# Kernel tuning notes

Hardware: AMD Instinct MI355X
Metric: run time of the kernel (lower is better)

Reference implementation:

```python
import jax, jax.numpy as jnp
import numpy as np

N = 100000   # nodes
E = 1600000  # edges
D = 128      # input_dim == hidden_dim
L = 3        # n_layers
P = 7        # n_properties
B = 64       # graphs in batch
BN_EPS = 1e-5
NEG_SLOPE = 0.2


def setup_inputs() -> dict:
    key = jax.random.key(0)
    ks = jax.random.split(key, 18)
    s = 1.0 / np.sqrt(D)
    sp = 1.0 / np.sqrt(P)
    return {
        "x": jax.random.normal(ks[0], (N, D), jnp.float32),
        "edge_index": jax.random.randint(ks[1], (2, E), 0, N, dtype=jnp.int64),
        "batch": jnp.sort(jax.random.randint(ks[2], (N,), 0, B, dtype=jnp.int64)),
        "graph_stats": jax.random.normal(ks[3], (B, P), jnp.float32),
        # GIN MLP params (stacked over layers; input_dim == hidden_dim == D)
        "W1s": jax.random.normal(ks[4], (L, D, D), jnp.float32) * s,
        "b1s": jnp.zeros((L, D), jnp.float32),
        "gammas": jnp.ones((L, D), jnp.float32),
        "betas": jnp.zeros((L, D), jnp.float32),
        "bn_means": jax.random.normal(ks[5], (L, D), jnp.float32) * 0.1,
        "bn_vars": jax.random.uniform(ks[6], (L, D), jnp.float32) + 0.5,
        "W2s": jax.random.normal(ks[7], (L, D, D), jnp.float32) * s,
        "b2s": jnp.zeros((L, D), jnp.float32),
        # stat conditioning transforms
        "statWs": jax.random.normal(ks[8], (L, P, D), jnp.float32) * sp,
        "statBs": jnp.zeros((L, D), jnp.float32),
        # fc_out
        "fcW": jax.random.normal(ks[9], (D, D), jnp.float32) * s,
        "fcB": jnp.zeros((D,), jnp.float32),
    }


def reference(x, edge_index, batch, graph_stats,
              W1s, b1s, gammas, betas, bn_means, bn_vars, W2s, b2s,
              statWs, statBs, fcW, fcB):
    # per-node graph stats (nan -> -100, then broadcast by graph id)
    node_stats = jnp.nan_to_num(graph_stats, nan=-100.0)[batch]  # [N, P]
    src, dst = edge_index[0], edge_index[1]
    h = x
    for i in range(L):
        # GIN aggregation (eps = 0): (1+eps)*h_i + sum_{j->i} h_j
        agg = jax.ops.segment_sum(h[src], dst, num_segments=N)  # [N, D]
        m = h + agg
        # MLP: Linear -> LeakyReLU(0.2) -> BatchNorm1d (eval) -> Linear -> LeakyReLU(0.2)
        m = jax.nn.leaky_relu(m @ W1s[i] + b1s[i], NEG_SLOPE)
        m = (m - bn_means[i]) * (gammas[i] / jnp.sqrt(bn_vars[i] + BN_EPS)) + betas[i]
        m = jax.nn.leaky_relu(m @ W2s[i] + b2s[i], NEG_SLOPE)
        # stats conditioning add (dropout is identity in eval mode)
        h = m + node_stats @ statWs[i] + statBs[i]
    return h @ fcW + fcB  # [N, D]
```

## Files before the change

### kernel.cpp

```cpp
#include <hip/hip_runtime.h>
#include <math.h>

#define N_NODES 100000
#define N_EDGES 1600000
#define D 128
#define L_LAYERS 3
#define P_STATS 7
#define B_GRAPHS 64
#define BN_EPS 1e-5f
#define NEG_SLOPE 0.2f

#define NB 196
#define BCAP 10240
#define EPB 6400

typedef __attribute__((ext_vector_type(8))) short bf16x8;
typedef __attribute__((ext_vector_type(4))) float f32x4;

static __device__ __forceinline__ short f2bf(float f) {
    union { float f; unsigned u; } v;
    v.f = f;
    unsigned r = v.u + 0x7fffu + ((v.u >> 16) & 1u);
    return (short)(r >> 16);
}

static __device__ __forceinline__ float bf2f(short s) {
    union { unsigned u; float f; } v;
    v.u = ((unsigned)(unsigned short)s) << 16;
    return v.f;
}


__global__ void zero_n_kernel(int* __restrict__ p, int n) {
    int i = blockIdx.x * blockDim.x + threadIdx.x;
    if (i < n) p[i] = 0;
}

__global__ __launch_bounds__(256) void bucketA_kernel(const int* __restrict__ src,
                                                      const int* __restrict__ dst,
                                                      int* __restrict__ bucket_cnt,
                                                      int2* __restrict__ bucketbuf) {
    __shared__ int s_src[EPB];
    __shared__ int s_dst[EPB];
    __shared__ int hist[NB], base[NB], loc[NB];
    const int tid = threadIdx.x;
    const int e0 = blockIdx.x * EPB;
    for (int i = tid; i < NB; i += 256) { hist[i] = 0; loc[i] = 0; }
    __syncthreads();
    for (int i = tid; i < EPB; i += 256) {
        int s = src[e0 + i];
        int d = dst[e0 + i];
        s_src[i] = s;
        s_dst[i] = d;
        atomicAdd(&hist[d >> 9], 1);
    }
    __syncthreads();
    for (int i = tid; i < NB; i += 256)
        base[i] = hist[i] ? atomicAdd(&bucket_cnt[i], hist[i]) : 0;
    __syncthreads();
    for (int i = tid; i < EPB; i += 256) {
        int d = s_dst[i];
        int b = d >> 9;
        int off = atomicAdd(&loc[b], 1);
        int idx = base[b] + off;
        if (idx < BCAP) bucketbuf[(size_t)b * BCAP + idx] = make_int2(s_src[i], d);
    }
}

__global__ __launch_bounds__(256) void bucketB1_kernel(const int* __restrict__ bucket_cnt,
                                                       const int2* __restrict__ bucketbuf,
                                                       int* __restrict__ deg) {
    __shared__ int hist[512];
    const int b = blockIdx.x;
    for (int i = threadIdx.x; i < 512; i += 256) hist[i] = 0;
    __syncthreads();
    int cnt = min(bucket_cnt[b], BCAP);
    for (int i = threadIdx.x; i < cnt; i += 256) {
        int d = bucketbuf[(size_t)b * BCAP + i].y;
        atomicAdd(&hist[d & 511], 1);
    }
    __syncthreads();
    int nbase = b << 9;
    for (int i = threadIdx.x; i < 512; i += 256) {
        int node = nbase + i;
        if (node < N_NODES) deg[node] = hist[i];
    }
}

__global__ __launch_bounds__(256) void bucketB2_kernel(const int* __restrict__ bucket_cnt,
                                                       const int2* __restrict__ bucketbuf,
                                                       int* __restrict__ cursor,
                                                       int* __restrict__ csr_src) {
    const int b = blockIdx.x;
    int cnt = min(bucket_cnt[b], BCAP);
    for (int i = threadIdx.x; i < cnt; i += 256) {
        int2 p = bucketbuf[(size_t)b * BCAP + i];
        int pos = atomicAdd(&cursor[p.y], 1);
        csr_src[pos] = p.x;
    }
}


__global__ void scan1_kernel(const int* __restrict__ deg, int* __restrict__ incl,
                             int* __restrict__ bsum) {
    __shared__ int s[256];
    const int tid = threadIdx.x;
    const int base = blockIdx.x * 2048;
    int v[8];
    int sum = 0;
    const int idx0 = base + tid * 8;
#pragma unroll
    for (int i = 0; i < 8; ++i) {
        int idx = idx0 + i;
        int d = (idx < N_NODES) ? deg[idx] : 0;
        sum += d;
        v[i] = sum;
    }
    s[tid] = sum;
    __syncthreads();
    for (int off = 1; off < 256; off <<= 1) {
        int t = (tid >= off) ? s[tid - off] : 0;
        __syncthreads();
        s[tid] += t;
        __syncthreads();
    }
    int prev = (tid > 0) ? s[tid - 1] : 0;
#pragma unroll
    for (int i = 0; i < 8; ++i) {
        int idx = idx0 + i;
        if (idx < N_NODES) incl[idx] = v[i] + prev;
    }
    if (tid == 255) bsum[blockIdx.x] = s[255];
}

__global__ void scan2_kernel(int* __restrict__ bsum, int nb) {
    if (threadIdx.x == 0 && blockIdx.x == 0) {
        int run = 0;
        for (int i = 0; i < nb; ++i) { int t = bsum[i]; bsum[i] = run; run += t; }
    }
}

__global__ void scan3_kernel(const int* __restrict__ deg, const int* __restrict__ incl,
                             const int* __restrict__ bsum, int* __restrict__ start,
                             int* __restrict__ cursor) {
    int i = blockIdx.x * blockDim.x + threadIdx.x;
    if (i < N_NODES) {
        int inc = incl[i] + bsum[i >> 11];
        int st = inc - deg[i];
        start[i] = st;
        cursor[i] = st;
    }
    if (i == 0) start[N_NODES] = N_EDGES;
}

__global__ void gproj_kernel(const float* __restrict__ gs, const float* __restrict__ statWs,
                             const float* __restrict__ statBs, float* __restrict__ gproj) {
    int b = blockIdx.x;
    int l = blockIdx.y;
    int j = threadIdx.x;
    float acc = statBs[l * D + j];
#pragma unroll
    for (int p = 0; p < P_STATS; ++p) {
        float g = gs[b * P_STATS + p];
        if (g != g) g = -100.0f;
        acc += g * statWs[(l * P_STATS + p) * D + j];
    }
    gproj[(l * B_GRAPHS + b) * D + j] = acc;
}

__global__ void wconv_kernel(const float* __restrict__ W1s, const float* __restrict__ W2s,
                             const float* __restrict__ fcW, short* __restrict__ wt) {
    int mid = blockIdx.y;
    const float* src = (mid < 3) ? (W1s + mid * D * D)
                                 : ((mid < 6) ? (W2s + (mid - 3) * D * D) : fcW);
    short* dstm = wt + mid * D * D;
    int i = blockIdx.x * 256 + threadIdx.x;
    int k = i >> 7, n = i & 127;
    dstm[n * D + k] = f2bf(src[i]);
}

__global__ __launch_bounds__(256) void xconv_kernel(const float* __restrict__ x,
                                                    short* __restrict__ xb) {
    int i = blockIdx.x * 256 + threadIdx.x;
    const float4* x4 = (const float4*)x;
    float4 a = x4[i * 2], b = x4[i * 2 + 1];
    short s[8];
    s[0] = f2bf(a.x); s[1] = f2bf(a.y); s[2] = f2bf(a.z); s[3] = f2bf(a.w);
    s[4] = f2bf(b.x); s[5] = f2bf(b.y); s[6] = f2bf(b.z); s[7] = f2bf(b.w);
    *(bf16x8*)&xb[i * 8] = *(bf16x8*)s;
}

__global__ __launch_bounds__(256) void agg_kernel(const short* __restrict__ hb,
                                                  const int* __restrict__ start,
                                                  const int* __restrict__ csr_src,
                                                  short* __restrict__ m_bf) {
    int node = blockIdx.x * 16 + (threadIdx.x >> 4);
    int c8 = threadIdx.x & 15;
    const bf16x8* h8 = (const bf16x8*)hb;

    bf16x8 own = h8[node * 16 + c8];
    float acc[8];
#pragma unroll
    for (int i = 0; i < 8; ++i) acc[i] = bf2f(own[i]);

    int s = start[node];
    int e = start[node + 1];
    int k = s;
    for (; k + 4 <= e; k += 4) {
        int sn0 = csr_src[k];
        int sn1 = csr_src[k + 1];
        int sn2 = csr_src[k + 2];
        int sn3 = csr_src[k + 3];
        bf16x8 v0 = h8[sn0 * 16 + c8];
        bf16x8 v1 = h8[sn1 * 16 + c8];
        bf16x8 v2 = h8[sn2 * 16 + c8];
        bf16x8 v3 = h8[sn3 * 16 + c8];
#pragma unroll
        for (int i = 0; i < 8; ++i) acc[i] += bf2f(v0[i]);
#pragma unroll
        for (int i = 0; i < 8; ++i) acc[i] += bf2f(v1[i]);
#pragma unroll
        for (int i = 0; i < 8; ++i) acc[i] += bf2f(v2[i]);
#pragma unroll
        for (int i = 0; i < 8; ++i) acc[i] += bf2f(v3[i]);
    }
    for (; k < e; ++k) {
        int sn0 = csr_src[k];
        bf16x8 v0 = h8[sn0 * 16 + c8];
#pragma unroll
        for (int i = 0; i < 8; ++i) acc[i] += bf2f(v0[i]);
    }

    short pk[8];
#pragma unroll
    for (int i = 0; i < 8; ++i) pk[i] = f2bf(acc[i]);
    *(bf16x8*)&m_bf[node * D + c8 * 8] = *(bf16x8*)pk;
}

template <bool FUSE_FC>
__global__ __launch_bounds__(256, 4) void mlp_mfma_kernel(
    const short* __restrict__ m_bf,
    const short* __restrict__ W1t,
    const float* __restrict__ b1,
    const float* __restrict__ gamma, const float* __restrict__ beta,
    const float* __restrict__ mean, const float* __restrict__ var,
    const short* __restrict__ W2t,
    const float* __restrict__ b2,
    const float* __restrict__ gproj, const int* __restrict__ batch,
    const short* __restrict__ Wft, const float* __restrict__ fcb,
    float* __restrict__ outf, short* __restrict__ outb) {
    __shared__ short sy[64 * 128];
    __shared__ float sB1[128], sSc[128], sSb[128], sB2[128], sFC[128];

    const int tid = threadIdx.x;
    const int wid = tid >> 6;
    const int lane = tid & 63;
    const int lr = lane & 15;
    const int lk = lane >> 4;

    if (tid < 128) {
        sB1[tid] = b1[tid];
        float sc = gamma[tid] * rsqrtf(var[tid] + BN_EPS);
        sSc[tid] = sc;
        sSb[tid] = beta[tid] - mean[tid] * sc;
        sB2[tid] = b2[tid];
        if (FUSE_FC) sFC[tid] = fcb[tid];
    }
    __syncthreads();

    const int nlBase = (wid >> 1) * 32;
    const int nodeBase = blockIdx.x * 64 + nlBase;
    const int featBase = (wid & 1) * 64;

    int nIdx[2];
#pragma unroll
    for (int mt = 0; mt < 2; ++mt) {
        int n = nodeBase + mt * 16 + lr;
        nIdx[mt] = (n < N_NODES) ? n : (N_NODES - 1);
    }

    f32x4 acc[4][2];
#pragma unroll
    for (int ft = 0; ft < 4; ++ft)
#pragma unroll
        for (int mt = 0; mt < 2; ++mt)
            acc[ft][mt] = (f32x4)(0.0f);

#pragma unroll
    for (int kt = 0; kt < 4; ++kt) {
        bf16x8 wfk[4];
#pragma unroll
        for (int ft = 0; ft < 4; ++ft)
            wfk[ft] = *(const bf16x8*)&W1t[(featBase + ft * 16 + lr) * D + kt * 32 + lk * 8];
        bf16x8 mf[2];
#pragma unroll
        for (int mt = 0; mt < 2; ++mt)
            mf[mt] = *(const bf16x8*)&m_bf[nIdx[mt] * D + kt * 32 + lk * 8];
#pragma unroll
        for (int ft = 0; ft < 4; ++ft)
#pragma unroll
            for (int mt = 0; mt < 2; ++mt)
                acc[ft][mt] = __builtin_amdgcn_mfma_f32_16x16x32_bf16(wfk[ft], mf[mt],
                                                                      acc[ft][mt], 0, 0, 0);
    }

#pragma unroll
    for (int ft = 0; ft < 4; ++ft) {
        int f0 = featBase + ft * 16 + lk * 4;
#pragma unroll
        for (int mt = 0; mt < 2; ++mt) {
            int nl = nlBase + mt * 16 + lr;
            short4 pk;
#pragma unroll
            for (int r = 0; r < 4; ++r) {
                float v = acc[ft][mt][r] + sB1[f0 + r];
                v = (v > 0.f) ? v : NEG_SLOPE * v;
                v = v * sSc[f0 + r] + sSb[f0 + r];
                ((short*)&pk)[r] = f2bf(v);
            }
            int byteoff = nl * 256 + f0 * 2;
            byteoff ^= (nl & 7) << 4;
            *(short4*)((char*)sy + byteoff) = pk;
        }
    }
    __syncthreads();

#pragma unroll
    for (int ft = 0; ft < 4; ++ft)
#pragma unroll
        for (int mt = 0; mt < 2; ++mt)
            acc[ft][mt] = (f32x4)(0.0f);

#pragma unroll
    for (int kt = 0; kt < 4; ++kt) {
        bf16x8 wfk[4];
#pragma unroll
        for (int ft = 0; ft < 4; ++ft)
            wfk[ft] = *(const bf16x8*)&W2t[(featBase + ft * 16 + lr) * D + kt * 32 + lk * 8];
        bf16x8 yf[2];
#pragma unroll
        for (int mt = 0; mt < 2; ++mt) {
            int nl = nlBase + mt * 16 + lr;
            int byteoff = nl * 256 + kt * 64 + lk * 16;
            byteoff ^= (nl & 7) << 4;
            yf[mt] = *(const bf16x8*)((char*)sy + byteoff);
        }
#pragma unroll
        for (int ft = 0; ft < 4; ++ft)
#pragma unroll
            for (int mt = 0; mt < 2; ++mt)
                acc[ft][mt] = __builtin_amdgcn_mfma_f32_16x16x32_bf16(wfk[ft], yf[mt],
                                                                      acc[ft][mt], 0, 0, 0);
    }

    __syncthreads();
#pragma unroll
    for (int ft = 0; ft < 4; ++ft) {
        int f0 = featBase + ft * 16 + lk * 4;
#pragma unroll
        for (int mt = 0; mt < 2; ++mt) {
            int nl = nlBase + mt * 16 + lr;
            int bid = batch[nIdx[mt]];
            const float4 gp = *(const float4*)&gproj[bid * D + f0];
            short4 pk;
            float v0 = acc[ft][mt][0] + sB2[f0 + 0]; v0 = (v0 > 0.f) ? v0 : NEG_SLOPE * v0; v0 += gp.x;
            float v1 = acc[ft][mt][1] + sB2[f0 + 1]; v1 = (v1 > 0.f) ? v1 : NEG_SLOPE * v1; v1 += gp.y;
            float v2 = acc[ft][mt][2] + sB2[f0 + 2]; v2 = (v2 > 0.f) ? v2 : NEG_SLOPE * v2; v2 += gp.z;
            float v3 = acc[ft][mt][3] + sB2[f0 + 3]; v3 = (v3 > 0.f) ? v3 : NEG_SLOPE * v3; v3 += gp.w;
            pk.x = f2bf(v0); pk.y = f2bf(v1); pk.z = f2bf(v2); pk.w = f2bf(v3);
            int byteoff = nl * 256 + f0 * 2;
            byteoff ^= (nl & 7) << 4;
            *(short4*)((char*)sy + byteoff) = pk;
        }
    }
    __syncthreads();

    if (!FUSE_FC) {
#pragma unroll
        for (int it = 0; it < 4; ++it) {
            int c = tid + it * 256;
            int nl = c >> 4;
            int c8 = c & 15;
            int node = blockIdx.x * 64 + nl;
            if (node < N_NODES) {
                int byteoff = nl * 256 + c8 * 16;
                byteoff ^= (nl & 7) << 4;
                bf16x8 v = *(const bf16x8*)((char*)sy + byteoff);
                *(bf16x8*)&outb[node * D + c8 * 8] = v;
            }
        }
        return;
    }

#pragma unroll
    for (int ft = 0; ft < 4; ++ft)
#pragma unroll
        for (int mt = 0; mt < 2; ++mt)
            acc[ft][mt] = (f32x4)(0.0f);

#pragma unroll
    for (int kt = 0; kt < 4; ++kt) {
        bf16x8 wfk[4];
#pragma unroll
        for (int ft = 0; ft < 4; ++ft)
            wfk[ft] = *(const bf16x8*)&Wft[(featBase + ft * 16 + lr) * D + kt * 32 + lk * 8];
        bf16x8 hf[2];
#pragma unroll
        for (int mt = 0; mt < 2; ++mt) {
            int nl = nlBase + mt * 16 + lr;
            int byteoff = nl * 256 + kt * 64 + lk * 16;
            byteoff ^= (nl & 7) << 4;
            hf[mt] = *(const bf16x8*)((char*)sy + byteoff);
        }
#pragma unroll
        for (int ft = 0; ft < 4; ++ft)
#pragma unroll
            for (int mt = 0; mt < 2; ++mt)
                acc[ft][mt] = __builtin_amdgcn_mfma_f32_16x16x32_bf16(wfk[ft], hf[mt],
                                                                      acc[ft][mt], 0, 0, 0);
    }

#pragma unroll
    for (int mt = 0; mt < 2; ++mt) {
        int node = nodeBase + mt * 16 + lr;
        if (node >= N_NODES) continue;
#pragma unroll
        for (int ft = 0; ft < 4; ++ft) {
            int f0 = featBase + ft * 16 + lk * 4;
            float4 o;
            o.x = acc[ft][mt][0] + sFC[f0 + 0];
            o.y = acc[ft][mt][1] + sFC[f0 + 1];
            o.z = acc[ft][mt][2] + sFC[f0 + 2];
            o.w = acc[ft][mt][3] + sFC[f0 + 3];
            *(float4*)&outf[node * D + f0] = o;
        }
    }
}


extern "C" void kernel_launch(void* const* d_in, const int* in_sizes, int n_in,
                              void* d_out, int out_size, void* d_ws, size_t ws_size,
                              hipStream_t stream) {
    const float* x = (const float*)d_in[0];
    const int* ei = (const int*)d_in[1];
    const int* src = ei;
    const int* dst = ei + N_EDGES;
    const int* batch = (const int*)d_in[2];
    const float* gs = (const float*)d_in[3];
    const float* W1s = (const float*)d_in[4];
    const float* b1s = (const float*)d_in[5];
    const float* gammas = (const float*)d_in[6];
    const float* betas = (const float*)d_in[7];
    const float* means = (const float*)d_in[8];
    const float* vars = (const float*)d_in[9];
    const float* W2s = (const float*)d_in[10];
    const float* b2s = (const float*)d_in[11];
    const float* statWs = (const float*)d_in[12];
    const float* statBs = (const float*)d_in[13];
    const float* fcW = (const float*)d_in[14];
    const float* fcB = (const float*)d_in[15];
    float* out = (float*)d_out;

    char* ws = (char*)d_ws;
    auto alloc = [&](size_t bytes) {
        char* p = ws;
        ws += (bytes + 255) / 256 * 256;
        return p;
    };
    int* deg = (int*)alloc(N_NODES * sizeof(int));
    int* incl = (int*)alloc(N_NODES * sizeof(int));
    int* bsum = (int*)alloc(64 * sizeof(int));
    int* start = (int*)alloc((N_NODES + 1) * sizeof(int));
    int* cursor = (int*)alloc(N_NODES * sizeof(int));
    int* csr_src = (int*)alloc(N_EDGES * sizeof(int));
    int* bucket_cnt = (int*)alloc(NB * sizeof(int));
    int2* bucketbuf = (int2*)alloc((size_t)NB * BCAP * sizeof(int2));
    float* gproj = (float*)alloc((size_t)L_LAYERS * B_GRAPHS * D * sizeof(float));
    short* wt = (short*)alloc((size_t)7 * D * D * sizeof(short));
    short* xb = (short*)alloc((size_t)N_NODES * D * sizeof(short));
    short* hb = (short*)alloc((size_t)N_NODES * D * sizeof(short));
    short* m_bf = (short*)alloc((size_t)N_NODES * D * sizeof(short));

    const int nscan = (N_NODES + 2047) / 2048;

    zero_n_kernel<<<1, 256, 0, stream>>>(bucket_cnt, NB);
    bucketA_kernel<<<N_EDGES / EPB, 256, 0, stream>>>(src, dst, bucket_cnt, bucketbuf);
    bucketB1_kernel<<<NB, 256, 0, stream>>>(bucket_cnt, bucketbuf, deg);
    scan1_kernel<<<nscan, 256, 0, stream>>>(deg, incl, bsum);
    scan2_kernel<<<1, 64, 0, stream>>>(bsum, nscan);
    scan3_kernel<<<(N_NODES + 255) / 256, 256, 0, stream>>>(deg, incl, bsum, start, cursor);
    bucketB2_kernel<<<NB, 256, 0, stream>>>(bucket_cnt, bucketbuf, cursor, csr_src);

    gproj_kernel<<<dim3(B_GRAPHS, L_LAYERS), D, 0, stream>>>(gs, statWs, statBs, gproj);
    wconv_kernel<<<dim3(64, 7), 256, 0, stream>>>(W1s, W2s, fcW, wt);
    xconv_kernel<<<(N_NODES * D / 8 + 255) / 256, 256, 0, stream>>>(x, xb);

    const int agg_blocks = N_NODES / 16;
    const int mlp_blocks = (N_NODES + 63) / 64;

    agg_kernel<<<agg_blocks, 256, 0, stream>>>(xb, start, csr_src, m_bf);
    mlp_mfma_kernel<false><<<mlp_blocks, 256, 0, stream>>>(
        m_bf, wt + 0 * D * D, b1s + 0 * D, gammas + 0 * D, betas + 0 * D, means + 0 * D,
        vars + 0 * D, wt + 3 * D * D, b2s + 0 * D, gproj + 0 * B_GRAPHS * D, batch,
        nullptr, nullptr, nullptr, hb);
    agg_kernel<<<agg_blocks, 256, 0, stream>>>(hb, start, csr_src, m_bf);
    mlp_mfma_kernel<false><<<mlp_blocks, 256, 0, stream>>>(
        m_bf, wt + 1 * D * D, b1s + 1 * D, gammas + 1 * D, betas + 1 * D, means + 1 * D,
        vars + 1 * D, wt + 4 * D * D, b2s + 1 * D, gproj + 1 * B_GRAPHS * D, batch,
        nullptr, nullptr, nullptr, hb);
    agg_kernel<<<agg_blocks, 256, 0, stream>>>(hb, start, csr_src, m_bf);
    mlp_mfma_kernel<true><<<mlp_blocks, 256, 0, stream>>>(
        m_bf, wt + 2 * D * D, b1s + 2 * D, gammas + 2 * D, betas + 2 * D, means + 2 * D,
        vars + 2 * D, wt + 5 * D * D, b2s + 2 * D, gproj + 2 * B_GRAPHS * D, batch,
        wt + 6 * D * D, fcB, out, nullptr);
}
```

Before: 412.5 us.

## Apply W1 before aggregation using linearity and fuse layer epilogue into gather

Uses linearity of the aggregation to compute h@W1 before the neighbour sum, so the gather kernel applies bias, LeakyReLU and BatchNorm directly and the MLP kernel only runs W2 plus the next layer's W1 (or fc). The initial x conversion is folded into a first GEMM kernel, and bucketA no longer stages edges in shared memory and reads src/dst twice instead. This removes one GEMM round-trip through shared memory per layer and the separate xconv pass. In exchange, sums are taken over bf16-rounded projected features, which changes rounding behaviour.

```diff
diff --git a/kernel.cpp b/kernel.cpp
--- a/kernel.cpp
+++ b/kernel.cpp
@@ -40,30 +40,26 @@
                                                       const int* __restrict__ dst,
                                                       int* __restrict__ bucket_cnt,
                                                       int2* __restrict__ bucketbuf) {
-    __shared__ int s_src[EPB];
-    __shared__ int s_dst[EPB];
     __shared__ int hist[NB], base[NB], loc[NB];
     const int tid = threadIdx.x;
     const int e0 = blockIdx.x * EPB;
     for (int i = tid; i < NB; i += 256) { hist[i] = 0; loc[i] = 0; }
     __syncthreads();
     for (int i = tid; i < EPB; i += 256) {
+        int d = dst[e0 + i];
+        atomicAdd(&hist[d >> 9], 1);
+    }
+    __syncthreads();
+    for (int i = tid; i < NB; i += 256)
+        base[i] = hist[i] ? atomicAdd(&bucket_cnt[i], hist[i]) : 0;
+    __syncthreads();
+    for (int i = tid; i < EPB; i += 256) {
         int s = src[e0 + i];
         int d = dst[e0 + i];
-        s_src[i] = s;
-        s_dst[i] = d;
-        atomicAdd(&hist[d >> 9], 1);
-    }
-    __syncthreads();
-    for (int i = tid; i < NB; i += 256)
-        base[i] = hist[i] ? atomicAdd(&bucket_cnt[i], hist[i]) : 0;
-    __syncthreads();
-    for (int i = tid; i < EPB; i += 256) {
-        int d = s_dst[i];
         int b = d >> 9;
         int off = atomicAdd(&loc[b], 1);
         int idx = base[b] + off;
-        if (idx < BCAP) bucketbuf[(size_t)b * BCAP + idx] = make_int2(s_src[i], d);
+        if (idx < BCAP) bucketbuf[(size_t)b * BCAP + idx] = make_int2(s, d);
     }
 }
 
@@ -179,26 +175,20 @@
     dstm[n * D + k] = f2bf(src[i]);
 }
 
-__global__ __launch_bounds__(256) void xconv_kernel(const float* __restrict__ x,
-                                                    short* __restrict__ xb) {
-    int i = blockIdx.x * 256 + threadIdx.x;
-    const float4* x4 = (const float4*)x;
-    float4 a = x4[i * 2], b = x4[i * 2 + 1];
-    short s[8];
-    s[0] = f2bf(a.x); s[1] = f2bf(a.y); s[2] = f2bf(a.z); s[3] = f2bf(a.w);
-    s[4] = f2bf(b.x); s[5] = f2bf(b.y); s[6] = f2bf(b.z); s[7] = f2bf(b.w);
-    *(bf16x8*)&xb[i * 8] = *(bf16x8*)s;
-}
-
-__global__ __launch_bounds__(256) void agg_kernel(const short* __restrict__ hb,
-                                                  const int* __restrict__ start,
-                                                  const int* __restrict__ csr_src,
-                                                  short* __restrict__ m_bf) {
+__global__ __launch_bounds__(256) void agg_ep_kernel(const short* __restrict__ g,
+                                                     const int* __restrict__ start,
+                                                     const int* __restrict__ csr_src,
+                                                     const float* __restrict__ b1,
+                                                     const float* __restrict__ gamma,
+                                                     const float* __restrict__ beta,
+                                                     const float* __restrict__ mean,
+                                                     const float* __restrict__ var,
+                                                     short* __restrict__ z) {
     int node = blockIdx.x * 16 + (threadIdx.x >> 4);
     int c8 = threadIdx.x & 15;
-    const bf16x8* h8 = (const bf16x8*)hb;
-
-    bf16x8 own = h8[node * 16 + c8];
+    const bf16x8* g8 = (const bf16x8*)g;
+
+    bf16x8 own = g8[node * 16 + c8];
     float acc[8];
 #pragma unroll
     for (int i = 0; i < 8; ++i) acc[i] = bf2f(own[i]);
@@ -211,10 +201,10 @@
         int sn1 = csr_src[k + 1];
         int sn2 = csr_src[k + 2];
         int sn3 = csr_src[k + 3];
-        bf16x8 v0 = h8[sn0 * 16 + c8];
-        bf16x8 v1 = h8[sn1 * 16 + c8];
-        bf16x8 v2 = h8[sn2 * 16 + c8];
-        bf16x8 v3 = h8[sn3 * 16 + c8];
+        bf16x8 v0 = g8[sn0 * 16 + c8];
+        bf16x8 v1 = g8[sn1 * 16 + c8];
+        bf16x8 v2 = g8[sn2 * 16 + c8];
+        bf16x8 v3 = g8[sn3 * 16 + c8];
 #pragma unroll
         for (int i = 0; i < 8; ++i) acc[i] += bf2f(v0[i]);
 #pragma unroll
@@ -226,48 +216,50 @@
     }
     for (; k < e; ++k) {
         int sn0 = csr_src[k];
-        bf16x8 v0 = h8[sn0 * 16 + c8];
+        bf16x8 v0 = g8[sn0 * 16 + c8];
 #pragma unroll
         for (int i = 0; i < 8; ++i) acc[i] += bf2f(v0[i]);
     }
 
+    const int f0 = c8 * 8;
+    float4 bb0 = *(const float4*)&b1[f0];
+    float4 bb1 = *(const float4*)&b1[f0 + 4];
+    float4 gm0 = *(const float4*)&gamma[f0];
+    float4 gm1 = *(const float4*)&gamma[f0 + 4];
+    float4 bt0 = *(const float4*)&beta[f0];
+    float4 bt1 = *(const float4*)&beta[f0 + 4];
+    float4 mn0 = *(const float4*)&mean[f0];
+    float4 mn1 = *(const float4*)&mean[f0 + 4];
+    float4 vr0 = *(const float4*)&var[f0];
+    float4 vr1 = *(const float4*)&var[f0 + 4];
+    float bbv[8] = {bb0.x, bb0.y, bb0.z, bb0.w, bb1.x, bb1.y, bb1.z, bb1.w};
+    float gmv[8] = {gm0.x, gm0.y, gm0.z, gm0.w, gm1.x, gm1.y, gm1.z, gm1.w};
+    float btv[8] = {bt0.x, bt0.y, bt0.z, bt0.w, bt1.x, bt1.y, bt1.z, bt1.w};
+    float mnv[8] = {mn0.x, mn0.y, mn0.z, mn0.w, mn1.x, mn1.y, mn1.z, mn1.w};
+    float vrv[8] = {vr0.x, vr0.y, vr0.z, vr0.w, vr1.x, vr1.y, vr1.z, vr1.w};
+
     short pk[8];
 #pragma unroll
-    for (int i = 0; i < 8; ++i) pk[i] = f2bf(acc[i]);
-    *(bf16x8*)&m_bf[node * D + c8 * 8] = *(bf16x8*)pk;
-}
-
-template <bool FUSE_FC>
-__global__ __launch_bounds__(256, 4) void mlp_mfma_kernel(
-    const short* __restrict__ m_bf,
-    const short* __restrict__ W1t,
-    const float* __restrict__ b1,
-    const float* __restrict__ gamma, const float* __restrict__ beta,
-    const float* __restrict__ mean, const float* __restrict__ var,
-    const short* __restrict__ W2t,
-    const float* __restrict__ b2,
-    const float* __restrict__ gproj, const int* __restrict__ batch,
-    const short* __restrict__ Wft, const float* __restrict__ fcb,
-    float* __restrict__ outf, short* __restrict__ outb) {
+    for (int i = 0; i < 8; ++i) {
+        float t = acc[i] + bbv[i];
+        t = (t > 0.f) ? t : NEG_SLOPE * t;
+        float sc = gmv[i] * rsqrtf(vrv[i] + BN_EPS);
+        t = t * sc + (btv[i] - mnv[i] * sc);
+        pk[i] = f2bf(t);
+    }
+    *(bf16x8*)&z[node * D + f0] = *(bf16x8*)pk;
+}
+
+__global__ __launch_bounds__(256, 4) void initgemm_kernel(const float* __restrict__ x,
+                                                          const short* __restrict__ Wt,
+                                                          short* __restrict__ g_out) {
     __shared__ short sy[64 * 128];
-    __shared__ float sB1[128], sSc[128], sSb[128], sB2[128], sFC[128];
-
     const int tid = threadIdx.x;
     const int wid = tid >> 6;
     const int lane = tid & 63;
     const int lr = lane & 15;
     const int lk = lane >> 4;
 
-    if (tid < 128) {
-        sB1[tid] = b1[tid];
-        float sc = gamma[tid] * rsqrtf(var[tid] + BN_EPS);
-        sSc[tid] = sc;
-        sSb[tid] = beta[tid] - mean[tid] * sc;
-        sB2[tid] = b2[tid];
-        if (FUSE_FC) sFC[tid] = fcb[tid];
-    }
-    __syncthreads();
-
     const int nlBase = (wid >> 1) * 32;
     const int nodeBase = blockIdx.x * 64 + nlBase;
     const int featBase = (wid & 1) * 64;
@@ -291,11 +283,17 @@
         bf16x8 wfk[4];
 #pragma unroll
         for (int ft = 0; ft < 4; ++ft)
-            wfk[ft] = *(const bf16x8*)&W1t[(featBase + ft * 16 + lr) * D + kt * 32 + lk * 8];
+            wfk[ft] = *(const bf16x8*)&Wt[(featBase + ft * 16 + lr) * D + kt * 32 + lk * 8];
         bf16x8 mf[2];
 #pragma unroll
-        for (int mt = 0; mt < 2; ++mt)
-            mf[mt] = *(const bf16x8*)&m_bf[nIdx[mt] * D + kt * 32 + lk * 8];
+        for (int mt = 0; mt < 2; ++mt) {
+            const float4* xp = (const float4*)&x[nIdx[mt] * D + kt * 32 + lk * 8];
+            float4 a = xp[0], b = xp[1];
+            short q[8];
+            q[0] = f2bf(a.x); q[1] = f2bf(a.y); q[2] = f2bf(a.z); q[3] = f2bf(a.w);
+            q[4] = f2bf(b.x); q[5] = f2bf(b.y); q[6] = f2bf(b.z); q[7] = f2bf(b.w);
+            mf[mt] = *(bf16x8*)q;
+        }
 #pragma unroll
         for (int ft = 0; ft < 4; ++ft)
 #pragma unroll
@@ -312,19 +310,64 @@
             int nl = nlBase + mt * 16 + lr;
             short4 pk;
 #pragma unroll
-            for (int r = 0; r < 4; ++r) {
-                float v = acc[ft][mt][r] + sB1[f0 + r];
-                v = (v > 0.f) ? v : NEG_SLOPE * v;
-                v = v * sSc[f0 + r] + sSb[f0 + r];
-                ((short*)&pk)[r] = f2bf(v);
-            }
+            for (int r = 0; r < 4; ++r) ((short*)&pk)[r] = f2bf(acc[ft][mt][r]);
             int byteoff = nl * 256 + f0 * 2;
             byteoff ^= (nl & 7) << 4;
             *(short4*)((char*)sy + byteoff) = pk;
         }
     }
     __syncthreads();
-
+#pragma unroll
+    for (int it = 0; it < 4; ++it) {
+        int c = tid + it * 256;
+        int nl = c >> 4;
+        int c8 = c & 15;
+        int node = blockIdx.x * 64 + nl;
+        if (node < N_NODES) {
+            int byteoff = nl * 256 + c8 * 16;
+            byteoff ^= (nl & 7) << 4;
+            bf16x8 v = *(const bf16x8*)((char*)sy + byteoff);
+            *(bf16x8*)&g_out[node * D + c8 * 8] = v;
+        }
+    }
+}
+
+template <bool FINAL>
+__global__ __launch_bounds__(256, 4) void mlp2_kernel(
+    const short* __restrict__ z,
+    const short* __restrict__ W2t,
+    const float* __restrict__ b2,
+    const float* __restrict__ gproj, const int* __restrict__ batch,
+    const short* __restrict__ Wnt,
+    const float* __restrict__ fcb,
+    float* __restrict__ outf, short* __restrict__ g_out) {
+    __shared__ short sy[64 * 128];
+    __shared__ float sB2[128], sFC[128];
+
+    const int tid = threadIdx.x;
+    const int wid = tid >> 6;
+    const int lane = tid & 63;
+    const int lr = lane & 15;
+    const int lk = lane >> 4;
+
+    if (tid < 128) {
+        sB2[tid] = b2[tid];
+        if (FINAL) sFC[tid] = fcb[tid];
+    }
+    __syncthreads();
+
+    const int nlBase = (wid >> 1) * 32;
+    const int nodeBase = blockIdx.x * 64 + nlBase;
+    const int featBase = (wid & 1) * 64;
+
+    int nIdx[2];
+#pragma unroll
+    for (int mt = 0; mt < 2; ++mt) {
+        int n = nodeBase + mt * 16 + lr;
+        nIdx[mt] = (n < N_NODES) ? n : (N_NODES - 1);
+    }
+
+    f32x4 acc[4][2];
 #pragma unroll
     for (int ft = 0; ft < 4; ++ft)
 #pragma unroll
@@ -337,23 +380,18 @@
 #pragma unroll
         for (int ft = 0; ft < 4; ++ft)
             wfk[ft] = *(const bf16x8*)&W2t[(featBase + ft * 16 + lr) * D + kt * 32 + lk * 8];
-        bf16x8 yf[2];
-#pragma unroll
-        for (int mt = 0; mt < 2; ++mt) {
-            int nl = nlBase + mt * 16 + lr;
-            int byteoff = nl * 256 + kt * 64 + lk * 16;
-            byteoff ^= (nl & 7) << 4;
-            yf[mt] = *(const bf16x8*)((char*)sy + byteoff);
-        }
+        bf16x8 zf[2];
+#pragma unroll
+        for (int mt = 0; mt < 2; ++mt)
+            zf[mt] = *(const bf16x8*)&z[nIdx[mt] * D + kt * 32 + lk * 8];
 #pragma unroll
         for (int ft = 0; ft < 4; ++ft)
 #pragma unroll
             for (int mt = 0; mt < 2; ++mt)
-                acc[ft][mt] = __builtin_amdgcn_mfma_f32_16x16x32_bf16(wfk[ft], yf[mt],
+                acc[ft][mt] = __builtin_amdgcn_mfma_f32_16x16x32_bf16(wfk[ft], zf[mt],
                                                                       acc[ft][mt], 0, 0, 0);
     }
 
-    __syncthreads();
 #pragma unroll
     for (int ft = 0; ft < 4; ++ft) {
         int f0 = featBase + ft * 16 + lk * 4;
@@ -375,23 +413,6 @@
     }
     __syncthreads();
 
-    if (!FUSE_FC) {
-#pragma unroll
-        for (int it = 0; it < 4; ++it) {
-            int c = tid + it * 256;
-            int nl = c >> 4;
-            int c8 = c & 15;
-            int node = blockIdx.x * 64 + nl;
-            if (node < N_NODES) {
-                int byteoff = nl * 256 + c8 * 16;
-                byteoff ^= (nl & 7) << 4;
-                bf16x8 v = *(const bf16x8*)((char*)sy + byteoff);
-                *(bf16x8*)&outb[node * D + c8 * 8] = v;
-            }
-        }
-        return;
-    }
-
 #pragma unroll
     for (int ft = 0; ft < 4; ++ft)
 #pragma unroll
@@ -403,7 +424,7 @@
         bf16x8 wfk[4];
 #pragma unroll
         for (int ft = 0; ft < 4; ++ft)
-            wfk[ft] = *(const bf16x8*)&Wft[(featBase + ft * 16 + lr) * D + kt * 32 + lk * 8];
+            wfk[ft] = *(const bf16x8*)&Wnt[(featBase + ft * 16 + lr) * D + kt * 32 + lk * 8];
         bf16x8 hf[2];
 #pragma unroll
         for (int mt = 0; mt < 2; ++mt) {
@@ -420,19 +441,52 @@
                                                                       acc[ft][mt], 0, 0, 0);
     }
 
-#pragma unroll
-    for (int mt = 0; mt < 2; ++mt) {
-        int node = nodeBase + mt * 16 + lr;
-        if (node >= N_NODES) continue;
-#pragma unroll
-        for (int ft = 0; ft < 4; ++ft) {
-            int f0 = featBase + ft * 16 + lk * 4;
-            float4 o;
-            o.x = acc[ft][mt][0] + sFC[f0 + 0];
-            o.y = acc[ft][mt][1] + sFC[f0 + 1];
-            o.z = acc[ft][mt][2] + sFC[f0 + 2];
-            o.w = acc[ft][mt][3] + sFC[f0 + 3];
-            *(float4*)&outf[node * D + f0] = o;
+    if (FINAL) {
+#pragma unroll
+        for (int mt = 0; mt < 2; ++mt) {
+            int node = nodeBase + mt * 16 + lr;
+            if (node >= N_NODES) continue;
+#pragma unroll
+            for (int ft = 0; ft < 4; ++ft) {
+                int f0 = featBase + ft * 16 + lk * 4;
+                float4 o;
+                o.x = acc[ft][mt][0] + sFC[f0 + 0];
+                o.y = acc[ft][mt][1] + sFC[f0 + 1];
+                o.z = acc[ft][mt][2] + sFC[f0 + 2];
+                o.w = acc[ft][mt][3] + sFC[f0 + 3];
+                *(float4*)&outf[node * D + f0] = o;
+            }
+        }
+        return;
+    }
+
+    __syncthreads();
+#pragma unroll
+    for (int ft = 0; ft < 4; ++ft) {
+        int f0 = featBase + ft * 16 + lk * 4;
+#pragma unroll
+        for (int mt = 0; mt < 2; ++mt) {
+            int nl = nlBase + mt * 16 + lr;
+            short4 pk;
+#pragma unroll
+            for (int r = 0; r < 4; ++r) ((short*)&pk)[r] = f2bf(acc[ft][mt][r]);
+            int byteoff = nl * 256 + f0 * 2;
+            byteoff ^= (nl & 7) << 4;
+            *(short4*)((char*)sy + byteoff) = pk;
+        }
+    }
+    __syncthreads();
+#pragma unroll
+    for (int it = 0; it < 4; ++it) {
+        int c = tid + it * 256;
+        int nl = c >> 4;
+        int c8 = c & 15;
+        int node = blockIdx.x * 64 + nl;
+        if (node < N_NODES) {
+            int byteoff = nl * 256 + c8 * 16;
+            byteoff ^= (nl & 7) << 4;
+            bf16x8 v = *(const bf16x8*)((char*)sy + byteoff);
+            *(bf16x8*)&g_out[node * D + c8 * 8] = v;
         }
     }
 }
@@ -477,9 +531,8 @@
     int2* bucketbuf = (int2*)alloc((size_t)NB * BCAP * sizeof(int2));
     float* gproj = (float*)alloc((size_t)L_LAYERS * B_GRAPHS * D * sizeof(float));
     short* wt = (short*)alloc((size_t)7 * D * D * sizeof(short));
-    short* xb = (short*)alloc((size_t)N_NODES * D * sizeof(short));
-    short* hb = (short*)alloc((size_t)N_NODES * D * sizeof(short));
-    short* m_bf = (short*)alloc((size_t)N_NODES * D * sizeof(short));
+    short* g_buf = (short*)alloc((size_t)N_NODES * D * sizeof(short));
+    short* z_buf = (short*)alloc((size_t)N_NODES * D * sizeof(short));
 
     const int nscan = (N_NODES + 2047) / 2048;
 
@@ -493,24 +546,28 @@
 
     gproj_kernel<<<dim3(B_GRAPHS, L_LAYERS), D, 0, stream>>>(gs, statWs, statBs, gproj);
     wconv_kernel<<<dim3(64, 7), 256, 0, stream>>>(W1s, W2s, fcW, wt);
-    xconv_kernel<<<(N_NODES * D / 8 + 255) / 256, 256, 0, stream>>>(x, xb);
 
     const int agg_blocks = N_NODES / 16;
     const int mlp_blocks = (N_NODES + 63) / 64;
 
-    agg_kernel<<<agg_blocks, 256, 0, stream>>>(xb, start, csr_src, m_bf);
-    mlp_mfma_kernel<false><<<mlp_blocks, 256, 0, stream>>>(
-        m_bf, wt + 0 * D * D, b1s + 0 * D, gammas + 0 * D, betas + 0 * D, means + 0 * D,
-        vars + 0 * D, wt + 3 * D * D, b2s + 0 * D, gproj + 0 * B_GRAPHS * D, batch,
-        nullptr, nullptr, nullptr, hb);
-    agg_kernel<<<agg_blocks, 256, 0, stream>>>(hb, start, csr_src, m_bf);
-    mlp_mfma_kernel<false><<<mlp_blocks, 256, 0, stream>>>(
-        m_bf, wt + 1 * D * D, b1s + 1 * D, gammas + 1 * D, betas + 1 * D, means + 1 * D,
-        vars + 1 * D, wt + 4 * D * D, b2s + 1 * D, gproj + 1 * B_GRAPHS * D, batch,
-        nullptr, nullptr, nullptr, hb);
-    agg_kernel<<<agg_blocks, 256, 0, stream>>>(hb, start, csr_src, m_bf);
-    mlp_mfma_kernel<true><<<mlp_blocks, 256, 0, stream>>>(
-        m_bf, wt + 2 * D * D, b1s + 2 * D, gammas + 2 * D, betas + 2 * D, means + 2 * D,
-        vars + 2 * D, wt + 5 * D * D, b2s + 2 * D, gproj + 2 * B_GRAPHS * D, batch,
+    initgemm_kernel<<<mlp_blocks, 256, 0, stream>>>(x, wt + 0 * D * D, g_buf);
+
+    agg_ep_kernel<<<agg_blocks, 256, 0, stream>>>(g_buf, start, csr_src, b1s + 0 * D,
+                                                  gammas + 0 * D, betas + 0 * D, means + 0 * D,
+                                                  vars + 0 * D, z_buf);
+    mlp2_kernel<false><<<mlp_blocks, 256, 0, stream>>>(
+        z_buf, wt + 3 * D * D, b2s + 0 * D, gproj + 0 * B_GRAPHS * D, batch,
+        wt + 1 * D * D, nullptr, nullptr, g_buf);
+    agg_ep_kernel<<<agg_blocks, 256, 0, stream>>>(g_buf, start, csr_src, b1s + 1 * D,
+                                                  gammas + 1 * D, betas + 1 * D, means + 1 * D,
+                                                  vars + 1 * D, z_buf);
+    mlp2_kernel<false><<<mlp_blocks, 256, 0, stream>>>(
+        z_buf, wt + 4 * D * D, b2s + 1 * D, gproj + 1 * B_GRAPHS * D, batch,
+        wt + 2 * D * D, nullptr, nullptr, g_buf);
+    agg_ep_kernel<<<agg_blocks, 256, 0, stream>>>(g_buf, start, csr_src, b1s + 2 * D,
+                                                  gammas + 2 * D, betas + 2 * D, means + 2 * D,
+                                                  vars + 2 * D, z_buf);
+    mlp2_kernel<true><<<mlp_blocks, 256, 0, stream>>>(
+        z_buf, wt + 5 * D * D, b2s + 2 * D, gproj + 2 * B_GRAPHS * D, batch,
         wt + 6 * D * D, fcB, out, nullptr);
 }
```

Measured after the change: 429.9 us. +4.2%, slower.
